# Performance work log

Measured on AMD Instinct MI355X. Metric: run time of the kernel, lower is better.

## Reference

```python
import jax, jax.numpy as jnp
import numpy as np

MUL = 64                  # multiplicity of 0e and 1o channels
N_NODES = 50000
N_EDGES = 500000
DIM_KEY = 32
FEAT = MUL * 4            # 64x0e (64) + 64x1o (192) = 256
# e3nn FullyConnectedTensorProduct(in, '10x0e', out) normalization:
# path_weight * w3j = 1/sqrt(mul_in * mul_z) = 1/sqrt(64*10)
INV640 = 1.0 / np.sqrt(MUL * 10)
ISQ3 = 1.0 / np.sqrt(3.0)   # w3j(1,1,0) = delta/sqrt(3)
ISQ2 = 1.0 / np.sqrt(2.0)   # path_weight sqrt(alpha) after 'element' norm (2 paths/out)


def _fctp(x, z, W0, W1):
    """FullyConnectedTensorProduct('64x0e+64x1o', '10x0e', '64x0e+64x1o').
    Scalars mix 0e block, vectors mix 1o block; w3j/path-weight factors reduce to 1/sqrt(640)."""
    x0 = x[:, :MUL]                       # (N, 64)
    x1 = x[:, MUL:].reshape(-1, MUL, 3)   # (N, 64, 3)
    o0 = jnp.einsum('nu,nv,uvw->nw', x0, z, W0) * INV640
    o1 = jnp.einsum('nuk,nv,uvw->nwk', x1, z, W1) * INV640
    return jnp.concatenate([o0, o1.reshape(-1, MUL * 3)], axis=-1)


def setup_inputs() -> dict:
    key = jax.random.key(0)
    ks = jax.random.split(key, 13)
    return {
        'x': jax.random.normal(ks[0], (N_NODES, FEAT), jnp.float32),
        'z': jax.random.normal(ks[1], (N_NODES, 10), jnp.float32),
        'edge_src': jax.random.randint(ks[2], (N_EDGES,), 0, N_NODES, jnp.int32),
        'edge_dst': jax.random.randint(ks[3], (N_EDGES,), 0, N_NODES, jnp.int32),
        'edge_len_emb': jax.random.normal(ks[4], (N_EDGES, DIM_KEY), jnp.float32),
        'edge_attr': jax.random.normal(ks[5], (N_EDGES, 4), jnp.float32),
        # learned params: four FCTPs (si, lin1, lin2 each have one 0e and one 1o path)
        'W_si0': jax.random.normal(ks[6], (MUL, 10, MUL), jnp.float32),
        'W_si1': jax.random.normal(ks[7], (MUL, 10, MUL), jnp.float32),
        'W_l1_0': jax.random.normal(ks[8], (MUL, 10, MUL), jnp.float32),
        'W_l1_1': jax.random.normal(ks[9], (MUL, 10, MUL), jnp.float32),
        'W_l2_0': jax.random.normal(ks[10], (MUL, 10, MUL), jnp.float32),
        'W_l2_1': jax.random.normal(ks[11], (MUL, 10, MUL), jnp.float32),
        # per-edge TP weights: 4 'uvu' paths x 64 = 256
        'tp_weight': jax.random.normal(ks[12], (DIM_KEY, 4 * MUL), jnp.float32),
    }


def reference(x, z, edge_src, edge_dst, edge_len_emb, edge_attr,
              W_si0, W_si1, W_l1_0, W_l1_1, W_l2_0, W_l2_1, tp_weight):
    n = x.shape[0]
    s = _fctp(x, z, W_si0, W_si1)          # self-interaction
    xl = _fctp(x, z, W_l1_0, W_l1_1)       # lin1

    w = edge_len_emb @ tp_weight           # (E, 256) per-edge TP weights
    w1, w2, w3, w4 = jnp.split(w, 4, axis=-1)  # instr order: 0ex0e->0e, 0ex1o->1o, 1ox0e->1o, 1ox1o->0e

    xs = xl[edge_src]                      # gather (E, 256)
    x0 = xs[:, :MUL]                       # (E, 64)
    x1 = xs[:, MUL:].reshape(-1, MUL, 3)   # (E, 64, 3)
    sh0 = edge_attr[:, 0:1]                # (E, 1) scalar SH
    sh1 = edge_attr[:, 1:4]                # (E, 3) vector SH

    # 'uvu' weighted tensor product (component norm, element path norm):
    # out_0e = sqrt(1/2) * [ w1*x0*sh0 + w4*(x1.sh1)/sqrt(3) ]
    e0 = ISQ2 * (w1 * x0 * sh0 + ISQ3 * w4 * jnp.einsum('euk,ek->eu', x1, sh1))
    # out_1o = sqrt(3/2)/sqrt(3) * [ w2*x0*sh1 + w3*x1*sh0 ]
    e1 = ISQ2 * (w2[:, :, None] * x0[:, :, None] * sh1[:, None, :]
                 + w3[:, :, None] * x1 * sh0[:, :, None])
    edge_out = jnp.concatenate([e0, e1.reshape(-1, MUL * 3)], axis=-1)  # (E, 256)

    # scatter-add messages to destination nodes
    agg = jnp.zeros((n, FEAT), edge_out.dtype).at[edge_dst].add(edge_out)

    x_out = _fctp(agg, z, W_l2_0, W_l2_1)  # lin2
    return s + x_out / 10
```

## Files before the change

### kernel.cpp

```cpp
#include <hip/hip_runtime.h>

#define MULT 64
#define FEATD 256
#define ZDIM 10

#define INV640f 0.03952847075210474f
#define ISQ2f   0.7071067811865476f
#define ISQ3f   0.5773502691896258f

typedef _Float16 f16_t;
typedef f16_t f16x8_t __attribute__((ext_vector_type(8)));
typedef f16_t f16x4_t __attribute__((ext_vector_type(4)));
typedef float f32x4_t __attribute__((ext_vector_type(4)));

__global__ __launch_bounds__(256) void transform_x2(
    const float* __restrict__ x, f16_t* __restrict__ Xs,
    f16_t* __restrict__ Xv, int N)
{
    int idx = blockIdx.x * 256 + threadIdx.x;
    if (idx >= N * MULT) return;
    int n = idx >> 6;
    int u = idx & 63;
    const float* row = x + (size_t)n * FEATD;
    Xs[idx] = (f16_t)row[u];
    const float* x1p = row + MULT + u * 3;
    Xv[((size_t)3 * n + 0) * MULT + u] = (f16_t)x1p[0];
    Xv[((size_t)3 * n + 1) * MULT + u] = (f16_t)x1p[1];
    Xv[((size_t)3 * n + 2) * MULT + u] = (f16_t)x1p[2];
}

__global__ __launch_bounds__(256) void zprep_kernel(
    const float* __restrict__ z, float* __restrict__ zt,
    float* __restrict__ ztv, int N)
{
    int n = blockIdx.x * 256 + threadIdx.x;
    if (n >= N) return;
    const float* zr = z + (size_t)n * ZDIM;
#pragma unroll
    for (int v = 0; v < ZDIM; ++v) {
        float val = zr[v] * INV640f;
        zt[(size_t)v * N + n] = val;
        float* p = ztv + (size_t)v * 3 * N + 3 * (size_t)n;
        p[0] = val; p[1] = val; p[2] = val;
    }
}

__global__ __launch_bounds__(256) void tpwprep_kernel(
    const float* __restrict__ tpw, f16_t* __restrict__ tpwt)
{
    int idx = blockIdx.x * 256 + threadIdx.x;
    if (idx >= 256 * 32) return;
    int c = idx >> 5, k = idx & 31;
    float s = (c < 192) ? ISQ2f : (ISQ2f * ISQ3f);
    tpwt[(size_t)c * 32 + k] = (f16_t)(tpw[(size_t)k * 256 + c] * s);
}

__global__ __launch_bounds__(256) void aggcvt_kernel(
    const float* __restrict__ a, f16_t* __restrict__ h, int n4)
{
    int i = blockIdx.x * 256 + threadIdx.x;
    if (i >= n4) return;
    float4 v = *(const float4*)(a + (size_t)i * 4);
    f16x4_t o;
    o[0] = (f16_t)v.x; o[1] = (f16_t)v.y; o[2] = (f16_t)v.z; o[3] = (f16_t)v.w;
    *(f16x4_t*)(h + (size_t)i * 4) = o;
}

__device__ __forceinline__ void preload_W(
    const float* __restrict__ W, int c0, int q, int mm, f16x8_t (&B)[20])
{
    const int col = c0 + mm;
#pragma unroll
    for (int ks = 0; ks < 20; ++ks) {
        const int v = ks >> 1;
        const int ub = ((ks & 1) << 5) + (q << 3);
        const int base = v * 64 + col;
#pragma unroll
        for (int j = 0; j < 8; ++j)
            B[ks][j] = (f16_t)W[(ub + j) * 640 + base];
    }
}

__global__ __launch_bounds__(256, 2) void fctp_pass_out(
    const f16_t* __restrict__ Xs, const f16_t* __restrict__ Xv,
    const float* __restrict__ zt, const float* __restrict__ ztv,
    const float* __restrict__ Wsi0, const float* __restrict__ Wsi1,
    float* __restrict__ out, int N, int nsc)
{
    const int lane = threadIdx.x & 63;
    const int wave = threadIdx.x >> 6;
    const int c0 = wave << 4;
    const int q = lane >> 4;
    const int mm = lane & 15;
    const bool sc = (int)blockIdx.x < nsc;
    const float* W = sc ? Wsi0 : Wsi1;
    const f16_t* Xsel = sc ? Xs : Xv;
    const float* ztb = sc ? zt : ztv;
    const size_t zsr = sc ? (size_t)N : (size_t)3 * N;
    const int ntiles = sc ? (N >> 4) : ((3 * N) >> 4);
    const int worker = sc ? (int)blockIdx.x : ((int)blockIdx.x - nsc);
    const int nworkers = sc ? nsc : 3 * nsc;

    f16x8_t B[20];
    preload_W(W, c0, q, mm, B);

    int tile = worker;
    if (tile >= ntiles) return;
    f16x8_t cxlo, cxhi;
    f32x4_t czq[ZDIM];
    {
        const int r = (tile << 4) + mm;
        cxlo = *(const f16x8_t*)(Xsel + ((size_t)r << 6) + (q << 3));
        cxhi = *(const f16x8_t*)(Xsel + ((size_t)r << 6) + 32 + (q << 3));
        const int rb4 = (tile << 4) + (q << 2);
#pragma unroll
        for (int v = 0; v < ZDIM; ++v)
            czq[v] = *(const f32x4_t*)(ztb + (size_t)v * zsr + rb4);
    }

    for (; tile < ntiles; tile += nworkers) {
        const int nt = tile + nworkers;
        f16x8_t nxlo = cxlo, nxhi = cxhi;
        f32x4_t nzq[ZDIM];
#pragma unroll
        for (int v = 0; v < ZDIM; ++v) nzq[v] = czq[v];
        if (nt < ntiles) {
            const int r = (nt << 4) + mm;
            nxlo = *(const f16x8_t*)(Xsel + ((size_t)r << 6) + (q << 3));
            nxhi = *(const f16x8_t*)(Xsel + ((size_t)r << 6) + 32 + (q << 3));
            const int nrb4 = (nt << 4) + (q << 2);
#pragma unroll
            for (int v = 0; v < ZDIM; ++v)
                nzq[v] = *(const f32x4_t*)(ztb + (size_t)v * zsr + nrb4);
        }
        __builtin_amdgcn_sched_barrier(0);

        const int rb4 = (tile << 4) + (q << 2);
        f32x4_t acc = {0.f, 0.f, 0.f, 0.f};
#pragma unroll
        for (int v = 0; v < ZDIM; ++v) {
            f32x4_t t = {0.f, 0.f, 0.f, 0.f};
            t = __builtin_amdgcn_mfma_f32_16x16x32_f16(cxlo, B[2 * v], t, 0, 0, 0);
            t = __builtin_amdgcn_mfma_f32_16x16x32_f16(cxhi, B[2 * v + 1], t, 0, 0, 0);
#pragma unroll
            for (int reg = 0; reg < 4; ++reg)
                acc[reg] = fmaf(czq[v][reg], t[reg], acc[reg]);
        }

        const int w = c0 + mm;
#pragma unroll
        for (int reg = 0; reg < 4; ++reg) {
            const int ro = rb4 + reg;
            if (sc) {
                out[(size_t)ro * FEATD + w] = acc[reg];
            } else {
                const unsigned nn = (unsigned)ro / 3u;
                const int k = ro - 3 * (int)nn;
                out[(size_t)nn * FEATD + MULT + w * 3 + k] = acc[reg];
            }
        }
        cxlo = nxlo; cxhi = nxhi;
#pragma unroll
        for (int v = 0; v < ZDIM; ++v) czq[v] = nzq[v];
    }
}

__global__ __launch_bounds__(256, 2) void fctp_pass_xl(
    const f16_t* __restrict__ Xs, const f16_t* __restrict__ Xv,
    const float* __restrict__ zt, const float* __restrict__ ztv,
    const float* __restrict__ Wl10, const float* __restrict__ Wl11,
    f16_t* __restrict__ xls, f16_t* __restrict__ xlv, int N, int nsc)
{
    const int lane = threadIdx.x & 63;
    const int wave = threadIdx.x >> 6;
    const int c0 = wave << 4;
    const int q = lane >> 4;
    const int mm = lane & 15;
    const bool sc = (int)blockIdx.x < nsc;
    const float* W = sc ? Wl10 : Wl11;
    const f16_t* Xsel = sc ? Xs : Xv;
    const float* ztb = sc ? zt : ztv;
    const size_t zsr = sc ? (size_t)N : (size_t)3 * N;
    const int ntiles = sc ? (N >> 4) : ((3 * N) >> 4);
    const int worker = sc ? (int)blockIdx.x : ((int)blockIdx.x - nsc);
    const int nworkers = sc ? nsc : 3 * nsc;

    f16x8_t B[20];
    preload_W(W, c0, q, mm, B);

    f16_t* Osel = sc ? xls : xlv;

    int tile = worker;
    if (tile >= ntiles) return;
    f16x8_t cxlo, cxhi;
    f32x4_t czq[ZDIM];
    {
        const int r = (tile << 4) + mm;
        cxlo = *(const f16x8_t*)(Xsel + ((size_t)r << 6) + (q << 3));
        cxhi = *(const f16x8_t*)(Xsel + ((size_t)r << 6) + 32 + (q << 3));
        const int rb4 = (tile << 4) + (q << 2);
#pragma unroll
        for (int v = 0; v < ZDIM; ++v)
            czq[v] = *(const f32x4_t*)(ztb + (size_t)v * zsr + rb4);
    }

    for (; tile < ntiles; tile += nworkers) {
        const int nt = tile + nworkers;
        f16x8_t nxlo = cxlo, nxhi = cxhi;
        f32x4_t nzq[ZDIM];
#pragma unroll
        for (int v = 0; v < ZDIM; ++v) nzq[v] = czq[v];
        if (nt < ntiles) {
            const int r = (nt << 4) + mm;
            nxlo = *(const f16x8_t*)(Xsel + ((size_t)r << 6) + (q << 3));
            nxhi = *(const f16x8_t*)(Xsel + ((size_t)r << 6) + 32 + (q << 3));
            const int nrb4 = (nt << 4) + (q << 2);
#pragma unroll
            for (int v = 0; v < ZDIM; ++v)
                nzq[v] = *(const f32x4_t*)(ztb + (size_t)v * zsr + nrb4);
        }
        __builtin_amdgcn_sched_barrier(0);

        const int rb4 = (tile << 4) + (q << 2);
        f32x4_t acc = {0.f, 0.f, 0.f, 0.f};
#pragma unroll
        for (int v = 0; v < ZDIM; ++v) {
            f32x4_t t = {0.f, 0.f, 0.f, 0.f};
            t = __builtin_amdgcn_mfma_f32_16x16x32_f16(cxlo, B[2 * v], t, 0, 0, 0);
            t = __builtin_amdgcn_mfma_f32_16x16x32_f16(cxhi, B[2 * v + 1], t, 0, 0, 0);
#pragma unroll
            for (int reg = 0; reg < 4; ++reg)
                acc[reg] = fmaf(czq[v][reg], t[reg], acc[reg]);
        }

        const int w = c0 + mm;
#pragma unroll
        for (int reg = 0; reg < 4; ++reg) {
            const int ro = rb4 + reg;
            Osel[((size_t)ro << 6) + w] = (f16_t)acc[reg];
        }
        cxlo = nxlo; cxhi = nxhi;
#pragma unroll
        for (int v = 0; v < ZDIM; ++v) czq[v] = nzq[v];
    }
}

__global__ __launch_bounds__(256, 2) void fctp_stageC_mfma(
    const f16_t* __restrict__ aggsh, const f16_t* __restrict__ aggvh,
    const float* __restrict__ zt, const float* __restrict__ ztv,
    const float* __restrict__ Wl20, const float* __restrict__ Wl21,
    float* __restrict__ out, int N, int nsc)
{
    const int lane = threadIdx.x & 63;
    const int wave = threadIdx.x >> 6;
    const int c0 = wave << 4;
    const int q = lane >> 4;
    const int mm = lane & 15;
    const bool sc = (int)blockIdx.x < nsc;
    const float* W = sc ? Wl20 : Wl21;
    const f16_t* Asel = sc ? aggsh : aggvh;
    const float* ztb = sc ? zt : ztv;
    const size_t zsr = sc ? (size_t)N : (size_t)3 * N;
    const int ntiles = sc ? (N >> 4) : ((3 * N) >> 4);
    const int worker = sc ? (int)blockIdx.x : ((int)blockIdx.x - nsc);
    const int nworkers = sc ? nsc : 3 * nsc;

    f16x8_t B[20];
    preload_W(W, c0, q, mm, B);

    int tile = worker;
    if (tile >= ntiles) return;
    f16x8_t cxlo, cxhi;
    f32x4_t czq[ZDIM];
    {
        const int r = (tile << 4) + mm;
        cxlo = *(const f16x8_t*)(Asel + ((size_t)r << 6) + (q << 3));
        cxhi = *(const f16x8_t*)(Asel + ((size_t)r << 6) + 32 + (q << 3));
        const int rb4 = (tile << 4) + (q << 2);
#pragma unroll
        for (int v = 0; v < ZDIM; ++v)
            czq[v] = *(const f32x4_t*)(ztb + (size_t)v * zsr + rb4);
    }

    for (; tile < ntiles; tile += nworkers) {
        const int nt = tile + nworkers;
        f16x8_t nxlo = cxlo, nxhi = cxhi;
        f32x4_t nzq[ZDIM];
#pragma unroll
        for (int v = 0; v < ZDIM; ++v) nzq[v] = czq[v];
        if (nt < ntiles) {
            const int r = (nt << 4) + mm;
            nxlo = *(const f16x8_t*)(Asel + ((size_t)r << 6) + (q << 3));
            nxhi = *(const f16x8_t*)(Asel + ((size_t)r << 6) + 32 + (q << 3));
            const int nrb4 = (nt << 4) + (q << 2);
#pragma unroll
            for (int v = 0; v < ZDIM; ++v)
                nzq[v] = *(const f32x4_t*)(ztb + (size_t)v * zsr + nrb4);
        }
        const int rb4 = (tile << 4) + (q << 2);
        const int w = c0 + mm;
        size_t oidx[4];
        float oold[4];
#pragma unroll
        for (int reg = 0; reg < 4; ++reg) {
            const int ro = rb4 + reg;
            if (sc) {
                oidx[reg] = (size_t)ro * FEATD + w;
            } else {
                const unsigned nn = (unsigned)ro / 3u;
                const int k = ro - 3 * (int)nn;
                oidx[reg] = (size_t)nn * FEATD + MULT + w * 3 + k;
            }
            oold[reg] = out[oidx[reg]];
        }
        __builtin_amdgcn_sched_barrier(0);

        f32x4_t acc = {0.f, 0.f, 0.f, 0.f};
#pragma unroll
        for (int v = 0; v < ZDIM; ++v) {
            f32x4_t t = {0.f, 0.f, 0.f, 0.f};
            t = __builtin_amdgcn_mfma_f32_16x16x32_f16(cxlo, B[2 * v], t, 0, 0, 0);
            t = __builtin_amdgcn_mfma_f32_16x16x32_f16(cxhi, B[2 * v + 1], t, 0, 0, 0);
#pragma unroll
            for (int reg = 0; reg < 4; ++reg)
                acc[reg] = fmaf(czq[v][reg], t[reg], acc[reg]);
        }

#pragma unroll
        for (int reg = 0; reg < 4; ++reg)
            out[oidx[reg]] = oold[reg] + acc[reg] * 0.1f;

        cxlo = nxlo; cxhi = nxhi;
#pragma unroll
        for (int v = 0; v < ZDIM; ++v) czq[v] = nzq[v];
    }
}

__global__ __launch_bounds__(256) void hist_kernel(
    const int* __restrict__ edst, int* __restrict__ cnt, int E)
{
    int e = blockIdx.x * 256 + threadIdx.x;
    if (e >= E) return;
    atomicAdd(&cnt[edst[e]], 1);
}

__global__ __launch_bounds__(1024) void scan_block(
    const int* __restrict__ cnt, int* __restrict__ off,
    int* __restrict__ bsum, int N)
{
    __shared__ int sh[1024];
    int tid = threadIdx.x;
    int i = blockIdx.x * 1024 + tid;
    int v = (i < N) ? cnt[i] : 0;
    sh[tid] = v;
    __syncthreads();
#pragma unroll
    for (int d = 1; d < 1024; d <<= 1) {
        int t = (tid >= d) ? sh[tid - d] : 0;
        __syncthreads();
        sh[tid] += t;
        __syncthreads();
    }
    if (i < N) off[i + 1] = sh[tid];
    if (tid == 1023) bsum[blockIdx.x] = sh[1023];
    if (i == 0) off[0] = 0;
}

__global__ __launch_bounds__(64) void scan_sums(int* __restrict__ bsum, int nb)
{
    int tid = threadIdx.x;
    int v = (tid < nb) ? bsum[tid] : 0;
#pragma unroll
    for (int d = 1; d < 64; d <<= 1) {
        int t = __shfl_up(v, d, 64);
        if (tid >= d) v += t;
    }
    int ex = __shfl_up(v, 1, 64);
    if (tid == 0) ex = 0;
    if (tid < nb) bsum[tid] = ex;
}

__global__ __launch_bounds__(1024) void scan_add(
    int* __restrict__ off, const int* __restrict__ bsum, int N)
{
    int i = blockIdx.x * 1024 + threadIdx.x;
    if (i < N) off[i + 1] += bsum[blockIdx.x];
}

__global__ __launch_bounds__(256) void scatter_kernel(
    const int* __restrict__ edst, const int* __restrict__ esrc,
    const float* __restrict__ eattr, const int* __restrict__ off,
    int* __restrict__ cursor, int* __restrict__ perm,
    int* __restrict__ sperm, float* __restrict__ eattr_p, int E)
{
    int e = blockIdx.x * 256 + threadIdx.x;
    if (e >= E) return;
    int d = edst[e];
    int pos = off[d] + atomicAdd(&cursor[d], 1);
    perm[pos] = e;
    sperm[pos] = esrc[e];
    float4 at = *(const float4*)(eattr + (size_t)e * 4);
    *(float4*)(eattr_p + (size_t)pos * 4) = at;
}

__global__ __launch_bounds__(256, 3) void aggregate6(
    const int* __restrict__ off, const int* __restrict__ sperm,
    const int* __restrict__ perm, const float* __restrict__ elem,
    const f16_t* __restrict__ tpwt, const float* __restrict__ eattr_p,
    const f16_t* __restrict__ xls, const f16_t* __restrict__ xlv,
    float* __restrict__ aggs, float* __restrict__ aggv, int N)
{
    __shared__ f16_t wtile[4][16 * 256];
    int n = (blockIdx.x * 256 + threadIdx.x) >> 6;
    if (n >= N) return;
    const int u = threadIdx.x & 63;
    const int wid = threadIdx.x >> 6;
    const int mm = u & 15, q = u >> 4;
    f16_t* wt = &wtile[wid][0];

    f16x8_t B[16];
#pragma unroll
    for (int s = 0; s < 16; ++s)
        B[s] = *(const f16x8_t*)(tpwt + ((size_t)(s * 16 + mm)) * 32 + q * 8);

    int cs0 = __builtin_amdgcn_readfirstlane(off[n]);
    int cs1 = __builtin_amdgcn_readfirstlane(off[n + 1]);

    float accx = 0.f, accy = 0.f, accz = 0.f, accw = 0.f;

    if (cs0 < cs1) {
        const int last = cs1 - 1;

        int sa = __builtin_amdgcn_readfirstlane(sperm[cs0]);
        float a_xs = (float)xls[((size_t)sa << 6) + u];
        float a_v0 = (float)xlv[((size_t)(3 * sa + 0) << 6) + u];
        float a_v1 = (float)xlv[((size_t)(3 * sa + 1) << 6) + u];
        float a_v2 = (float)xlv[((size_t)(3 * sa + 2) << 6) + u];
        int ib = (cs0 + 1 <= last) ? cs0 + 1 : last;
        int sb = __builtin_amdgcn_readfirstlane(sperm[ib]);
        float b_xs = (float)xls[((size_t)sb << 6) + u];
        float b_v0 = (float)xlv[((size_t)(3 * sb + 0) << 6) + u];
        float b_v1 = (float)xlv[((size_t)(3 * sb + 1) << 6) + u];
        float b_v2 = (float)xlv[((size_t)(3 * sb + 2) << 6) + u];

        int i = cs0;
        for (int g = cs0; g < cs1; g += 16) {
            const int gend = (g + 16 < cs1) ? g + 16 : cs1;

            int pos = g + mm; if (pos > last) pos = last;
            int e = perm[pos];
            const float* er = elem + ((size_t)e << 5) + q * 8;
            float4 ea = *(const float4*)er;
            float4 eb = *(const float4*)(er + 4);
            f16x8_t A;
            A[0] = (f16_t)ea.x; A[1] = (f16_t)ea.y; A[2] = (f16_t)ea.z; A[3] = (f16_t)ea.w;
            A[4] = (f16_t)eb.x; A[5] = (f16_t)eb.y; A[6] = (f16_t)eb.z; A[7] = (f16_t)eb.w;

#pragma unroll
            for (int t = 0; t < 4; ++t) {
                f32x4_t D0 = {0.f, 0.f, 0.f, 0.f}, D1 = {0.f, 0.f, 0.f, 0.f};
                f32x4_t D2 = {0.f, 0.f, 0.f, 0.f}, D3 = {0.f, 0.f, 0.f, 0.f};
                D0 = __builtin_amdgcn_mfma_f32_16x16x32_f16(A, B[t],      D0, 0, 0, 0);
                D1 = __builtin_amdgcn_mfma_f32_16x16x32_f16(A, B[4 + t],  D1, 0, 0, 0);
                D2 = __builtin_amdgcn_mfma_f32_16x16x32_f16(A, B[8 + t],  D2, 0, 0, 0);
                D3 = __builtin_amdgcn_mfma_f32_16x16x32_f16(A, B[12 + t], D3, 0, 0, 0);
#pragma unroll
                for (int reg = 0; reg < 4; ++reg) {
                    const int row = (q << 2) + reg;
                    f16x4_t wq;
                    wq[0] = (f16_t)D0[reg];
                    wq[1] = (f16_t)D1[reg];
                    wq[2] = (f16_t)D2[reg];
                    wq[3] = (f16_t)D3[reg];
                    *(f16x4_t*)(wt + ((size_t)(row * 64 + (t * 16 + mm)) << 2)) = wq;
                }
            }

            while (i < gend) {
                {
                    f16x4_t wq = *(const f16x4_t*)(wt + ((size_t)((i - g) * 64 + u) << 2));
                    float w1 = (float)wq[0], w2 = (float)wq[1], w3 = (float)wq[2], w4 = (float)wq[3];
                    float4 at = *(const float4*)(eattr_p + ((size_t)i << 2));
                    float dot3 = a_v0 * at.y + a_v1 * at.z + a_v2 * at.w;
                    accx = fmaf(w1 * a_xs, at.x, accx);
                    accx = fmaf(w4, dot3, accx);
                    float w2x = w2 * a_xs;
                    accy = fmaf(w2x, at.y, accy);
                    accz = fmaf(w2x, at.z, accz);
                    accw = fmaf(w2x, at.w, accw);
                    float w3s = w3 * at.x;
                    accy = fmaf(w3s, a_v0, accy);
                    accz = fmaf(w3s, a_v1, accz);
                    accw = fmaf(w3s, a_v2, accw);
                }
                {
                    int inx = (i + 2 <= last) ? i + 2 : last;
                    int sn = __builtin_amdgcn_readfirstlane(sperm[inx]);
                    a_xs = (float)xls[((size_t)sn << 6) + u];
                    a_v0 = (float)xlv[((size_t)(3 * sn + 0) << 6) + u];
                    a_v1 = (float)xlv[((size_t)(3 * sn + 1) << 6) + u];
                    a_v2 = (float)xlv[((size_t)(3 * sn + 2) << 6) + u];
                }
                if (++i >= gend) break;
                {
                    f16x4_t wq = *(const f16x4_t*)(wt + ((size_t)((i - g) * 64 + u) << 2));
                    float w1 = (float)wq[0], w2 = (float)wq[1], w3 = (float)wq[2], w4 = (float)wq[3];
                    float4 at = *(const float4*)(eattr_p + ((size_t)i << 2));
                    float dot3 = b_v0 * at.y + b_v1 * at.z + b_v2 * at.w;
                    accx = fmaf(w1 * b_xs, at.x, accx);
                    accx = fmaf(w4, dot3, accx);
                    float w2x = w2 * b_xs;
                    accy = fmaf(w2x, at.y, accy);
                    accz = fmaf(w2x, at.z, accz);
                    accw = fmaf(w2x, at.w, accw);
                    float w3s = w3 * at.x;
                    accy = fmaf(w3s, b_v0, accy);
                    accz = fmaf(w3s, b_v1, accz);
                    accw = fmaf(w3s, b_v2, accw);
                }
                {
                    int inx = (i + 2 <= last) ? i + 2 : last;
                    int sn = __builtin_amdgcn_readfirstlane(sperm[inx]);
                    b_xs = (float)xls[((size_t)sn << 6) + u];
                    b_v0 = (float)xlv[((size_t)(3 * sn + 0) << 6) + u];
                    b_v1 = (float)xlv[((size_t)(3 * sn + 1) << 6) + u];
                    b_v2 = (float)xlv[((size_t)(3 * sn + 2) << 6) + u];
                }
                ++i;
            }
        }
    }

    aggs[((size_t)n << 6) + u] = accx;
    aggv[((size_t)(3 * n + 0) << 6) + u] = accy;
    aggv[((size_t)(3 * n + 1) << 6) + u] = accz;
    aggv[((size_t)(3 * n + 2) << 6) + u] = accw;
}

extern "C" void kernel_launch(void* const* d_in, const int* in_sizes, int n_in,
                              void* d_out, int out_size, void* d_ws, size_t ws_size,
                              hipStream_t stream)
{
    const float* x     = (const float*)d_in[0];
    const float* z     = (const float*)d_in[1];
    const int*   esrc  = (const int*)d_in[2];
    const int*   edst  = (const int*)d_in[3];
    const float* elem  = (const float*)d_in[4];
    const float* eattr = (const float*)d_in[5];
    const float* Wsi0  = (const float*)d_in[6];
    const float* Wsi1  = (const float*)d_in[7];
    const float* Wl10  = (const float*)d_in[8];
    const float* Wl11  = (const float*)d_in[9];
    const float* Wl20  = (const float*)d_in[10];
    const float* Wl21  = (const float*)d_in[11];
    const float* tpw   = (const float*)d_in[12];
    float* out = (float*)d_out;

    const int N = in_sizes[1] / ZDIM;
    const int E = in_sizes[2];
    const int Ehalf = E / 2;

    f16_t* xls  = (f16_t*)d_ws;
    f16_t* xlv  = xls + (size_t)N * 64;
    float* aggs = (float*)(xlv + (size_t)3 * N * 64);
    float* aggv = aggs + (size_t)N * 64;
    char*  R    = (char*)(aggv + (size_t)3 * N * 64);
    f16_t* Xs   = (f16_t*)R;
    f16_t* Xv   = Xs + (size_t)N * 64;
    f16_t* aggh = (f16_t*)R;
    size_t Rbytes = (size_t)Ehalf * 256 * sizeof(f16_t);
    float* eattr_p = (float*)(R + Rbytes);
    int*   sperm   = (int*)(eattr_p + (size_t)E * 4);
    int*   perm    = sperm + E;
    int*   cnt     = perm + E;
    int*   cursor  = cnt + N;
    int*   off     = cursor + N;
    int*   bsum    = off + (N + 1);
    size_t zoff = (((size_t)(bsum + 64) - (size_t)d_ws) + 255) & ~(size_t)255;
    float* zt  = (float*)((char*)d_ws + zoff);
    float* ztv = zt + (size_t)10 * N;
    f16_t* tpwt = (f16_t*)(ztv + (size_t)30 * N);

    const int SCAN_B = 1024;
    int nb = (N + SCAN_B - 1) / SCAN_B;

    hipMemsetAsync(cnt, 0, 2 * (size_t)N * sizeof(int), stream);

    int g0 = (N * MULT + 255) / 256;
    hipLaunchKernelGGL(transform_x2, dim3(g0), dim3(256), 0, stream, x, Xs, Xv, N);
    int gz = (N + 255) / 256;
    hipLaunchKernelGGL(zprep_kernel, dim3(gz), dim3(256), 0, stream, z, zt, ztv, N);
    hipLaunchKernelGGL(tpwprep_kernel, dim3(32), dim3(256), 0, stream, tpw, tpwt);

    hipLaunchKernelGGL(fctp_pass_xl, dim3(512), dim3(256), 0, stream,
                       Xs, Xv, zt, ztv, Wl10, Wl11, xls, xlv, N, 128);
    hipLaunchKernelGGL(fctp_pass_out, dim3(512), dim3(256), 0, stream,
                       Xs, Xv, zt, ztv, Wsi0, Wsi1, out, N, 128);

    int geh = (E + 255) / 256;
    hipLaunchKernelGGL(hist_kernel, dim3(geh), dim3(256), 0, stream,
                       edst, cnt, E);
    hipLaunchKernelGGL(scan_block, dim3(nb), dim3(SCAN_B), 0, stream,
                       cnt, off, bsum, N);
    hipLaunchKernelGGL(scan_sums, dim3(1), dim3(64), 0, stream, bsum, nb);
    hipLaunchKernelGGL(scan_add, dim3(nb), dim3(SCAN_B), 0, stream,
                       off, bsum, N);
    hipLaunchKernelGGL(scatter_kernel, dim3(geh), dim3(256), 0, stream,
                       edst, esrc, eattr, off, cursor, perm, sperm, eattr_p, E);

    int ga = (N * 64 + 255) / 256;
    hipLaunchKernelGGL(aggregate6, dim3(ga), dim3(256), 0, stream,
                       off, sperm, perm, elem, tpwt, eattr_p, xls, xlv,
                       aggs, aggv, N);

    int n4 = N * 64;
    int gc = (n4 + 255) / 256;
    hipLaunchKernelGGL(aggcvt_kernel, dim3(gc), dim3(256), 0, stream,
                       aggs, aggh, n4);
    hipLaunchKernelGGL(fctp_stageC_mfma, dim3(512), dim3(256), 0, stream,
                       aggh, aggh + (size_t)N * 64, zt, ztv, Wl20, Wl21,
                       out, N, 128);
}
```

Before: 508.7 us.

## Interleave lin1 outputs per channel and deepen gather prefetch to four edges

```diff
diff --git a/kernel.cpp b/kernel.cpp
--- a/kernel.cpp
+++ b/kernel.cpp
@@ -169,7 +169,7 @@
     const f16_t* __restrict__ Xs, const f16_t* __restrict__ Xv,
     const float* __restrict__ zt, const float* __restrict__ ztv,
     const float* __restrict__ Wl10, const float* __restrict__ Wl11,
-    f16_t* __restrict__ xls, f16_t* __restrict__ xlv, int N, int nsc)
+    f16_t* __restrict__ xli, int N, int nsc)
 {
     const int lane = threadIdx.x & 63;
     const int wave = threadIdx.x >> 6;
@@ -188,8 +188,6 @@
     f16x8_t B[20];
     preload_W(W, c0, q, mm, B);
 
-    f16_t* Osel = sc ? xls : xlv;
-
     int tile = worker;
     if (tile >= ntiles) return;
     f16x8_t cxlo, cxhi;
@@ -237,7 +235,13 @@
 #pragma unroll
         for (int reg = 0; reg < 4; ++reg) {
             const int ro = rb4 + reg;
-            Osel[((size_t)ro << 6) + w] = (f16_t)acc[reg];
+            if (sc) {
+                xli[((size_t)ro * 64 + w) * 4 + 0] = (f16_t)acc[reg];
+            } else {
+                const unsigned nn = (unsigned)ro / 3u;
+                const int k = ro - 3 * (int)nn;
+                xli[((size_t)nn * 64 + w) * 4 + 1 + k] = (f16_t)acc[reg];
+            }
         }
         cxlo = nxlo; cxhi = nxhi;
 #pragma unroll
@@ -407,7 +411,7 @@
     const int* __restrict__ off, const int* __restrict__ sperm,
     const int* __restrict__ perm, const float* __restrict__ elem,
     const f16_t* __restrict__ tpwt, const float* __restrict__ eattr_p,
-    const f16_t* __restrict__ xls, const f16_t* __restrict__ xlv,
+    const f16_t* __restrict__ xli,
     float* __restrict__ aggs, float* __restrict__ aggv, int N)
 {
     __shared__ f16_t wtile[4][16 * 256];
@@ -431,17 +435,42 @@
     if (cs0 < cs1) {
         const int last = cs1 - 1;
 
-        int sa = __builtin_amdgcn_readfirstlane(sperm[cs0]);
-        float a_xs = (float)xls[((size_t)sa << 6) + u];
-        float a_v0 = (float)xlv[((size_t)(3 * sa + 0) << 6) + u];
-        float a_v1 = (float)xlv[((size_t)(3 * sa + 1) << 6) + u];
-        float a_v2 = (float)xlv[((size_t)(3 * sa + 2) << 6) + u];
-        int ib = (cs0 + 1 <= last) ? cs0 + 1 : last;
-        int sb = __builtin_amdgcn_readfirstlane(sperm[ib]);
-        float b_xs = (float)xls[((size_t)sb << 6) + u];
-        float b_v0 = (float)xlv[((size_t)(3 * sb + 0) << 6) + u];
-        float b_v1 = (float)xlv[((size_t)(3 * sb + 1) << 6) + u];
-        float b_v2 = (float)xlv[((size_t)(3 * sb + 2) << 6) + u];
+        f16x4_t xa, xb, xc, xd;
+        {
+            int i1 = (cs0 + 1 <= last) ? cs0 + 1 : last;
+            int i2 = (cs0 + 2 <= last) ? cs0 + 2 : last;
+            int i3 = (cs0 + 3 <= last) ? cs0 + 3 : last;
+            int s0 = __builtin_amdgcn_readfirstlane(sperm[cs0]);
+            int s1 = __builtin_amdgcn_readfirstlane(sperm[i1]);
+            int s2 = __builtin_amdgcn_readfirstlane(sperm[i2]);
+            int s3 = __builtin_amdgcn_readfirstlane(sperm[i3]);
+            xa = *(const f16x4_t*)(xli + (((size_t)s0 << 6) + u) * 4);
+            xb = *(const f16x4_t*)(xli + (((size_t)s1 << 6) + u) * 4);
+            xc = *(const f16x4_t*)(xli + (((size_t)s2 << 6) + u) * 4);
+            xd = *(const f16x4_t*)(xli + (((size_t)s3 << 6) + u) * 4);
+        }
+
+#define CONSUME_TP(X) { \
+        f16x4_t wq = *(const f16x4_t*)(wt + ((size_t)((i - g) * 64 + u) << 2)); \
+        float w1 = (float)wq[0], w2 = (float)wq[1], w3 = (float)wq[2], w4 = (float)wq[3]; \
+        float4 at = *(const float4*)(eattr_p + ((size_t)i << 2)); \
+        float xs = (float)X[0], v0 = (float)X[1], v1 = (float)X[2], v2 = (float)X[3]; \
+        float dot3 = v0 * at.y + v1 * at.z + v2 * at.w; \
+        accx = fmaf(w1 * xs, at.x, accx); \
+        accx = fmaf(w4, dot3, accx); \
+        float w2x = w2 * xs; \
+        accy = fmaf(w2x, at.y, accy); \
+        accz = fmaf(w2x, at.z, accz); \
+        accw = fmaf(w2x, at.w, accw); \
+        float w3s = w3 * at.x; \
+        accy = fmaf(w3s, v0, accy); \
+        accz = fmaf(w3s, v1, accz); \
+        accw = fmaf(w3s, v2, accw); }
+
+#define REFILL_TP(X) { \
+        int inx = (i + 4 <= last) ? i + 4 : last; \
+        int sn = __builtin_amdgcn_readfirstlane(sperm[inx]); \
+        X = *(const f16x4_t*)(xli + (((size_t)sn << 6) + u) * 4); }
 
         int i = cs0;
         for (int g = cs0; g < cs1; g += 16) {
@@ -477,58 +506,14 @@
             }
 
             while (i < gend) {
-                {
-                    f16x4_t wq = *(const f16x4_t*)(wt + ((size_t)((i - g) * 64 + u) << 2));
-                    float w1 = (float)wq[0], w2 = (float)wq[1], w3 = (float)wq[2], w4 = (float)wq[3];
-                    float4 at = *(const float4*)(eattr_p + ((size_t)i << 2));
-                    float dot3 = a_v0 * at.y + a_v1 * at.z + a_v2 * at.w;
-                    accx = fmaf(w1 * a_xs, at.x, accx);
-                    accx = fmaf(w4, dot3, accx);
-                    float w2x = w2 * a_xs;
-                    accy = fmaf(w2x, at.y, accy);
-                    accz = fmaf(w2x, at.z, accz);
-                    accw = fmaf(w2x, at.w, accw);
-                    float w3s = w3 * at.x;
-                    accy = fmaf(w3s, a_v0, accy);
-                    accz = fmaf(w3s, a_v1, accz);
-                    accw = fmaf(w3s, a_v2, accw);
-                }
-                {
-                    int inx = (i + 2 <= last) ? i + 2 : last;
-                    int sn = __builtin_amdgcn_readfirstlane(sperm[inx]);
-                    a_xs = (float)xls[((size_t)sn << 6) + u];
-                    a_v0 = (float)xlv[((size_t)(3 * sn + 0) << 6) + u];
-                    a_v1 = (float)xlv[((size_t)(3 * sn + 1) << 6) + u];
-                    a_v2 = (float)xlv[((size_t)(3 * sn + 2) << 6) + u];
-                }
-                if (++i >= gend) break;
-                {
-                    f16x4_t wq = *(const f16x4_t*)(wt + ((size_t)((i - g) * 64 + u) << 2));
-                    float w1 = (float)wq[0], w2 = (float)wq[1], w3 = (float)wq[2], w4 = (float)wq[3];
-                    float4 at = *(const float4*)(eattr_p + ((size_t)i << 2));
-                    float dot3 = b_v0 * at.y + b_v1 * at.z + b_v2 * at.w;
-                    accx = fmaf(w1 * b_xs, at.x, accx);
-                    accx = fmaf(w4, dot3, accx);
-                    float w2x = w2 * b_xs;
-                    accy = fmaf(w2x, at.y, accy);
-                    accz = fmaf(w2x, at.z, accz);
-                    accw = fmaf(w2x, at.w, accw);
-                    float w3s = w3 * at.x;
-                    accy = fmaf(w3s, b_v0, accy);
-                    accz = fmaf(w3s, b_v1, accz);
-                    accw = fmaf(w3s, b_v2, accw);
-                }
-                {
-                    int inx = (i + 2 <= last) ? i + 2 : last;
-                    int sn = __builtin_amdgcn_readfirstlane(sperm[inx]);
-                    b_xs = (float)xls[((size_t)sn << 6) + u];
-                    b_v0 = (float)xlv[((size_t)(3 * sn + 0) << 6) + u];
-                    b_v1 = (float)xlv[((size_t)(3 * sn + 1) << 6) + u];
-                    b_v2 = (float)xlv[((size_t)(3 * sn + 2) << 6) + u];
-                }
-                ++i;
+                CONSUME_TP(xa); REFILL_TP(xa); if (++i >= gend) break;
+                CONSUME_TP(xb); REFILL_TP(xb); if (++i >= gend) break;
+                CONSUME_TP(xc); REFILL_TP(xc); if (++i >= gend) break;
+                CONSUME_TP(xd); REFILL_TP(xd); ++i;
             }
         }
+#undef CONSUME_TP
+#undef REFILL_TP
     }
 
     aggs[((size_t)n << 6) + u] = accx;
@@ -560,9 +545,8 @@
     const int E = in_sizes[2];
     const int Ehalf = E / 2;
 
-    f16_t* xls  = (f16_t*)d_ws;
-    f16_t* xlv  = xls + (size_t)N * 64;
-    float* aggs = (float*)(xlv + (size_t)3 * N * 64);
+    f16_t* xli  = (f16_t*)d_ws;
+    float* aggs = (float*)(xli + (size_t)4 * N * 64);
     float* aggv = aggs + (size_t)N * 64;
     char*  R    = (char*)(aggv + (size_t)3 * N * 64);
     f16_t* Xs   = (f16_t*)R;
@@ -593,7 +577,7 @@
     hipLaunchKernelGGL(tpwprep_kernel, dim3(32), dim3(256), 0, stream, tpw, tpwt);
 
     hipLaunchKernelGGL(fctp_pass_xl, dim3(512), dim3(256), 0, stream,
-                       Xs, Xv, zt, ztv, Wl10, Wl11, xls, xlv, N, 128);
+                       Xs, Xv, zt, ztv, Wl10, Wl11, xli, N, 128);
     hipLaunchKernelGGL(fctp_pass_out, dim3(512), dim3(256), 0, stream,
                        Xs, Xv, zt, ztv, Wsi0, Wsi1, out, N, 128);
 
@@ -610,7 +594,7 @@
 
     int ga = (N * 64 + 255) / 256;
     hipLaunchKernelGGL(aggregate6, dim3(ga), dim3(256), 0, stream,
-                       off, sperm, perm, elem, tpwt, eattr_p, xls, xlv,
+                       off, sperm, perm, elem, tpwt, eattr_p, xli,
                        aggs, aggv, N);
 
     int n4 = N * 64;
```

After: 505.8 us. No clear change (-0.6%).
